# Optimization experiments

Measured on AMD Instinct MI355X. Metric: run time of the kernel, lower is better.

Reference implementation:

```python
import jax, jax.numpy as jnp
import numpy as np

B, S, C = 16, 2048, 512
E = S            # embed_dim == seq_len (RMSNorm applied on transposed seq axis)
H = 4 * E        # FFN hidden
LAMBDA_INIT = float(0.8 - 0.6 * np.exp(-0.3 * 1.0))  # layer_index = 1
SCALE = E ** (-0.25)
K = 5            # decomposition moving-average kernel


def rmsnorm(x, w, eps=1e-8):
    return x * jax.lax.rsqrt(jnp.mean(x * x, axis=-1, keepdims=True) + eps) * w


def decompose(a):
    # DLinear-style series decomposition: replicate-padded moving average along seq
    pad = (K - 1) // 2
    ap = jnp.concatenate([jnp.repeat(a[:, :1], pad, axis=1), a, jnp.repeat(a[:, -1:], pad, axis=1)], axis=1)
    n = a.shape[1]
    trend = sum(ap[:, i:i + n] for i in range(K)) / K
    return trend, a - trend


def setup_inputs() -> dict:
    key = jax.random.key(0)
    ks = jax.random.split(key, 12)
    p = lambda i, shape, s=0.02: jax.random.normal(ks[i], shape, jnp.float32) * s
    return {
        "x": jax.random.normal(ks[0], (B, S, C), jnp.float32),
        "ln_attn_w": jnp.ones((E,), jnp.float32),
        "q12_w": p(1, (E, 2 * E)), "q12_b": jnp.zeros((2 * E,), jnp.float32),
        "k12_w": p(2, (E, 2 * E)), "k12_b": jnp.zeros((2 * E,), jnp.float32),
        "v_w": p(3, (E, E)), "v_b": jnp.zeros((E,), jnp.float32),
        "lambda_q1": p(4, (E,), 0.1), "lambda_k1": p(5, (E,), 0.1),
        "lambda_q2": p(6, (E,), 0.1), "lambda_k2": p(7, (E,), 0.1),
        "norm_w": jnp.ones((E,), jnp.float32),
        "ln_ff_w": jnp.ones((E,), jnp.float32),
        "ff_w1": p(8, (E, H)), "ff_b1": jnp.zeros((H,), jnp.float32),
        "ff_w2": p(9, (H, E)), "ff_b2": jnp.zeros((E,), jnp.float32),
    }


def reference(x, ln_attn_w, q12_w, q12_b, k12_w, k12_b, v_w, v_b,
              lambda_q1, lambda_k1, lambda_q2, lambda_k2,
              norm_w, ln_ff_w, ff_w1, ff_b1, ff_w2, ff_b2):
    # pre-attention RMSNorm over the seq axis (via transpose)
    a = jnp.swapaxes(rmsnorm(jnp.swapaxes(x, -1, -2), ln_attn_w), -1, -2)  # [B,S,C]
    trend, seasonal = decompose(a)
    # project seq dim of trend/seasonal (iTransformer style: channels are tokens)
    q = jnp.swapaxes(trend, -1, -2) @ q12_w + q12_b      # [B,C,2S]
    q1, q2 = jnp.split(q, 2, axis=-1)                    # [B,C,S] each
    k = jnp.swapaxes(seasonal, -1, -2) @ k12_w + k12_b   # [B,C,2S]
    k1, k2 = jnp.split(k, 2, axis=-1)                    # [B,C,S]
    v = jnp.swapaxes(a, -1, -2) @ v_w + v_b              # [B,C,S]
    a1 = jnp.einsum('bis,bjs->bij', q1, k1) * SCALE      # [B,C,C]
    a2 = jnp.einsum('bis,bjs->bij', q2, k2) * SCALE      # [B,C,C]
    lam = jnp.exp(jnp.sum(lambda_q1 * lambda_k1)) - jnp.exp(jnp.sum(lambda_q2 * lambda_k2)) + LAMBDA_INIT
    d = jax.nn.softmax(a1, axis=-1) - lam * jax.nn.softmax(a2, axis=-1)
    attn = rmsnorm(d @ v, norm_w) * (1.0 - LAMBDA_INIT)  # [B,C,S]
    x = x + jnp.swapaxes(attn, -1, -2)
    # FFN over the seq axis
    h = rmsnorm(jnp.swapaxes(x, -1, -2), ln_ff_w)        # [B,C,S]
    ff = jax.nn.gelu(h @ ff_w1 + ff_b1, approximate=False) @ ff_w2 + ff_b2
    return x + jnp.swapaxes(ff, -1, -2)
```

## Files before the change

kernel.cpp:

```cpp
#include <hip/hip_runtime.h>
#include <hip/hip_bf16.h>

#define B_ 16
#define S_ 2048
#define C_ 512
#define H_ 8192

#define LAMBDA_INIT_F 0.3555090675909693f
#define ONE_M_LI_F    0.6444909324090307f
#define SCALE_F       0.14865088937534013f

using bf16x8 = __attribute__((ext_vector_type(8))) short;
using f32x4  = __attribute__((ext_vector_type(4))) float;

__device__ __forceinline__ float b2f(ushort u) {
  union { unsigned u; float f; } x; x.u = ((unsigned)u) << 16; return x.f;
}
__device__ __forceinline__ ushort f2b(float f) {
  union { float f; unsigned u; } x; x.f = f;
  unsigned r = x.u + 0x7fffu + ((x.u >> 16) & 1u);
  return (ushort)(r >> 16);
}

__device__ __forceinline__ void load_lds16(const void* g, void* s) {
  __builtin_amdgcn_global_load_lds((const __attribute__((address_space(1))) void*)g,
                                   (__attribute__((address_space(3))) void*)s,
                                   16, 0, 0);
}

#define WAITV8() asm volatile("s_waitcnt vmcnt(8)" ::: "memory")
#define WAITV4() asm volatile("s_waitcnt vmcnt(4)" ::: "memory")
#define WAITV0() asm volatile("s_waitcnt vmcnt(0)" ::: "memory")
#define WAITL0() do { asm volatile("s_waitcnt lgkmcnt(0)" ::: "memory"); __builtin_amdgcn_sched_barrier(0); } while (0)
#define BAR()    __builtin_amdgcn_s_barrier()

template <int EPI>
__global__ __launch_bounds__(512, 1) void gemm256(
    const ushort* __restrict__ A, const ushort* __restrict__ Bt,
    ushort* __restrict__ C, const float* __restrict__ bias,
    const ushort* __restrict__ addm,
    int K, int lda, int ldb, int ldc)
{
  __shared__ ushort lds[65536];
  const int t = threadIdx.x, w = t >> 6, lane = t & 63;
  const int fr = lane & 15, khl = lane >> 4;
  const int wr = w >> 2, wc = w & 3;

  const int gx = gridDim.x, gy = gridDim.y;
  const int id = blockIdx.y * gx + blockIdx.x;
  const int xcd = id & 7, l = id >> 3;
  const int tnb = (gy == 16) ? 3 : 2;
  const int lm = l >> tnb, ln = l & ((1 << tnb) - 1);
  const int m0 = ((xcd & 3) * 8 + lm) * 256;
  const int n0 = ((xcd >> 2) * (1 << tnb) + ln) * 256;

  const int sl    = (t & 7) ^ ((t >> 3) & 7);
  const int rbase = ((t >> 3) << 1) + (sl >> 2);
  const int khs   = sl & 3;
  const size_t aoff = (size_t)(m0 + rbase) * lda + khs * 8;
  const size_t boff = (size_t)(n0 + rbase) * ldb + khs * 8;
  const size_t jstA = (size_t)128 * lda, jstB = (size_t)128 * ldb;

  int ao[8], bo[4];
#pragma unroll
  for (int m = 0; m < 8; ++m) {
    const int row = wr * 128 + m * 16 + fr, dr = row >> 1;
    const int so = (((row & 1) << 2) + khl) ^ (dr & 7);
    ao[m] = dr * 64 + so * 8;
  }
#pragma unroll
  for (int n = 0; n < 4; ++n) {
    const int row = wc * 64 + n * 16 + fr, dr = row >> 1;
    const int so = (((row & 1) << 2) + khl) ^ (dr & 7);
    bo[n] = 8192 + dr * 64 + so * 8;
  }

  f32x4 acc[8][4] = {};
  const int U = K >> 5;

#define STAGE_U(u) do { \
    const ushort* sa_ = A  + aoff + (size_t)(u) * 32; \
    const ushort* sb_ = Bt + boff + (size_t)(u) * 32; \
    ushort* da_ = &lds[((u) & 3) * 16384 + w * 512]; \
    load_lds16(sa_, da_); load_lds16(sa_ + jstA, da_ + 4096); \
    load_lds16(sb_, da_ + 8192); load_lds16(sb_ + jstB, da_ + 12288); } while (0)
#define LDFRAG(u) do { const int sb_ = ((u) & 3) * 16384; \
    _Pragma("unroll") for (int m_ = 0; m_ < 8; ++m_) af[m_] = *(const bf16x8*)&lds[sb_ + ao[m_]]; \
    _Pragma("unroll") for (int n_ = 0; n_ < 4; ++n_) bg[n_] = *(const bf16x8*)&lds[sb_ + bo[n_]]; } while (0)
#define MFMA32() do { __builtin_amdgcn_s_setprio(1); \
    _Pragma("unroll") for (int m_ = 0; m_ < 8; ++m_) \
    _Pragma("unroll") for (int n_ = 0; n_ < 4; ++n_) \
      acc[m_][n_] = __builtin_amdgcn_mfma_f32_16x16x32_bf16(af[m_], bg[n_], acc[m_][n_], 0, 0, 0); \
    __builtin_amdgcn_s_setprio(0); } while (0)

  STAGE_U(0); STAGE_U(1); STAGE_U(2);
  WAITV8(); BAR();

  bf16x8 af[8], bg[4];
#pragma unroll 4
  for (int u = 0; u <= U - 4; ++u) {
    LDFRAG(u);
    STAGE_U(u + 3);
    WAITL0();
    MFMA32();
    WAITV8();
    BAR();
  }
  {
    LDFRAG(U - 3);
    WAITL0();
    MFMA32();
    WAITV4();
    BAR();
  }
  {
    LDFRAG(U - 2);
    WAITL0();
    MFMA32();
    WAITV0();
    BAR();
  }
  {
    LDFRAG(U - 1);
    WAITL0();
    MFMA32();
  }
#undef STAGE_U
#undef LDFRAG
#undef MFMA32

  const int r0 = khl * 4;
#pragma unroll
  for (int m = 0; m < 8; ++m)
#pragma unroll
    for (int nf = 0; nf < 4; ++nf) {
      const int gr = m0 + wr * 128 + m * 16 + r0;
      const int gc = n0 + wc * 64 + nf * 16 + fr;
      const float bb = (EPI == 3) ? 0.f : bias[gc];
#pragma unroll
      for (int r = 0; r < 4; ++r) {
        const size_t idx = (size_t)(gr + r) * ldc + gc;
        float v = acc[m][nf][r];
        if constexpr (EPI == 1) v += bb;
        if constexpr (EPI == 2) { v += bb; v = 0.5f * v * (1.f + erff(v * 0.7071067811865475f)); }
        if constexpr (EPI == 4) v += bb + b2f(addm[idx]) + b2f(C[idx]);
        C[idx] = f2b(v);
      }
    }
}

template <int EPI>
__global__ __launch_bounds__(256, 2) void gemm_nt(
    const ushort* __restrict__ Aall, const ushort* __restrict__ Ball,
    void* __restrict__ Call, int K, int lda, int ldb, int ldc,
    long sA, long sB, long sC, long sA2, long sB2, float alpha)
{
  __shared__ ushort lA[4096];
  __shared__ ushort lB[4096];
  const int t = threadIdx.x;
  const int m0 = blockIdx.x * 128, n0 = blockIdx.y * 128;
  const int zb = blockIdx.z & 15, zh = blockIdx.z >> 4;
  const ushort* A  = Aall + (size_t)zb * sA + (size_t)zh * sA2;
  const ushort* Bt = Ball + (size_t)zb * sB + (size_t)zh * sB2;
  const int lane = t & 63;
  const int wave = t >> 6;
  const int wm = (wave >> 1) * 64, wn = (wave & 1) * 64;
  const int fr = lane & 15, kh = lane >> 4;
  f32x4 acc[4][4] = {};
  const int srow = t >> 2;
  const int scol = (t & 3) * 8;
  const size_t ar0 = (size_t)(m0 + srow) * lda + scol;
  const size_t ar1 = (size_t)(m0 + 64 + srow) * lda + scol;
  const size_t br0 = (size_t)(n0 + srow) * ldb + scol;
  const size_t br1 = (size_t)(n0 + 64 + srow) * ldb + scol;
  const int wbase = wave * 512;

  for (int k0 = 0; k0 < K; k0 += 32) {
    __syncthreads();
    load_lds16(A + ar0 + k0,  &lA[wbase]);
    load_lds16(A + ar1 + k0,  &lA[2048 + wbase]);
    load_lds16(Bt + br0 + k0, &lB[wbase]);
    load_lds16(Bt + br1 + k0, &lB[2048 + wbase]);
    __syncthreads();
    bf16x8 af[4], bg[4];
#pragma unroll
    for (int i = 0; i < 4; ++i)
      af[i] = *(const bf16x8*)&lA[(wm + i * 16 + fr) * 32 + kh * 8];
#pragma unroll
    for (int j = 0; j < 4; ++j)
      bg[j] = *(const bf16x8*)&lB[(wn + j * 16 + fr) * 32 + kh * 8];
#pragma unroll
    for (int i = 0; i < 4; ++i)
#pragma unroll
      for (int j = 0; j < 4; ++j)
        acc[i][j] = __builtin_amdgcn_mfma_f32_16x16x32_bf16(af[i], bg[j], acc[i][j], 0, 0, 0);
  }

  const int r0 = kh * 4;
  if constexpr (EPI == 0) {
    float* C = (float*)Call + (size_t)blockIdx.z * sC;
#pragma unroll
    for (int i = 0; i < 4; ++i)
#pragma unroll
      for (int j = 0; j < 4; ++j) {
        const int gr = m0 + wm + i * 16 + r0;
        const int gc = n0 + wn + j * 16 + fr;
#pragma unroll
        for (int r = 0; r < 4; ++r)
          C[(size_t)(gr + r) * ldc + gc] = acc[i][j][r] * alpha;
      }
  } else {
    ushort* C = (ushort*)Call + (size_t)blockIdx.z * sC;
#pragma unroll
    for (int i = 0; i < 4; ++i)
#pragma unroll
      for (int j = 0; j < 4; ++j) {
        const int gr = m0 + wm + i * 16 + r0;
        const int gc = n0 + wn + j * 16 + fr;
#pragma unroll
        for (int r = 0; r < 4; ++r)
          C[(size_t)(gr + r) * ldc + gc] = f2b(acc[i][j][r] * alpha);
      }
  }
}

__device__ __forceinline__ float block_sum(float v, float* red) {
#pragma unroll
  for (int o = 32; o > 0; o >>= 1) v += __shfl_down(v, o, 64);
  __syncthreads();
  if ((threadIdx.x & 63) == 0) red[threadIdx.x >> 6] = v;
  __syncthreads();
  return red[0] + red[1] + red[2] + red[3];
}
__device__ __forceinline__ float block_max(float v, float* red) {
#pragma unroll
  for (int o = 32; o > 0; o >>= 1) v = fmaxf(v, __shfl_down(v, o, 64));
  __syncthreads();
  if ((threadIdx.x & 63) == 0) red[threadIdx.x >> 6] = v;
  __syncthreads();
  return fmaxf(fmaxf(red[0], red[1]), fmaxf(red[2], red[3]));
}

__global__ __launch_bounds__(256) void k_rms_part(const float* __restrict__ x, float* __restrict__ part) {
  const int c = blockIdx.x * 256 + threadIdx.x;
  const int sl = blockIdx.y;
  const int b = blockIdx.z;
  const float* p = x + (size_t)b * S_ * C_ + c;
  const int s0 = sl * 256;
  float s = 0.f;
  for (int i = 0; i < 256; ++i) { float v = p[(size_t)(s0 + i) * C_]; s += v * v; }
  part[((size_t)b * C_ + c) * 8 + sl] = s;
}
__global__ __launch_bounds__(256) void k_rms_fin(const float* __restrict__ part, float* __restrict__ rms1) {
  const int i = blockIdx.x * 256 + threadIdx.x;
  const float* p = part + (size_t)i * 8;
  float s = 0.f;
#pragma unroll
  for (int j = 0; j < 8; ++j) s += p[j];
  rms1[i] = rsqrtf(s * (1.f / S_) + 1e-8f);
}

__global__ __launch_bounds__(256) void k_trans_norm(const float* __restrict__ x, const float* __restrict__ rms1,
                                                    const float* __restrict__ w,
                                                    ushort* __restrict__ aT, ushort* __restrict__ xT) {
  __shared__ float tile[32][33];
  const int s0 = blockIdx.x * 32, c0 = blockIdx.y * 32, b = blockIdx.z;
  const int tx = threadIdx.x, ty = threadIdx.y;
  const float* xb = x + (size_t)b * S_ * C_;
#pragma unroll
  for (int r = 0; r < 4; ++r) {
    const int s = ty + 8 * r;
    tile[s][tx] = xb[(size_t)(s0 + s) * C_ + c0 + tx];
  }
  __syncthreads();
#pragma unroll
  for (int r = 0; r < 4; ++r) {
    const int c = ty + 8 * r;
    const float v = tile[tx][c];
    const float rm = rms1[b * C_ + c0 + c];
    const size_t o = ((size_t)b * C_ + c0 + c) * S_ + s0 + tx;
    xT[o] = f2b(v);
    aT[o] = f2b(v * rm * w[s0 + tx]);
  }
}

__global__ __launch_bounds__(256) void k_wtrans(const float* __restrict__ W, ushort* __restrict__ WT,
                                                int Kd, int Ndstride, int n_base) {
  __shared__ float tile[32][33];
  const int k0 = blockIdx.x * 32, n0 = blockIdx.y * 32;
  const int tx = threadIdx.x, ty = threadIdx.y;
#pragma unroll
  for (int r = 0; r < 4; ++r) {
    const int k = ty + 8 * r;
    tile[k][tx] = W[(size_t)(k0 + k) * Ndstride + n_base + n0 + tx];
  }
  __syncthreads();
#pragma unroll
  for (int r = 0; r < 4; ++r) {
    const int n = ty + 8 * r;
    WT[(size_t)(n0 + n) * Kd + k0 + tx] = f2b(tile[tx][n]);
  }
}

__global__ __launch_bounds__(256) void k_bt(const ushort* __restrict__ in, ushort* __restrict__ out, int R, int CL) {
  __shared__ ushort tile[32][33];
  const int r0 = blockIdx.x * 32, c0 = blockIdx.y * 32;
  const size_t zb = (size_t)blockIdx.z * R * CL;
  const int tx = threadIdx.x, ty = threadIdx.y;
#pragma unroll
  for (int r = 0; r < 4; ++r) {
    const int rr = ty + 8 * r;
    tile[rr][tx] = in[zb + (size_t)(r0 + rr) * CL + c0 + tx];
  }
  __syncthreads();
#pragma unroll
  for (int r = 0; r < 4; ++r) {
    const int cc = ty + 8 * r;
    out[zb + (size_t)(c0 + cc) * R + r0 + tx] = tile[tx][cc];
  }
}

__device__ __forceinline__ float trend5(const ushort* p, int s) {
  float sum = 0.f;
#pragma unroll
  for (int d = -2; d <= 2; ++d) {
    int ss = s + d; ss = ss < 0 ? 0 : (ss > S_ - 1 ? S_ - 1 : ss);
    sum += b2f(p[ss]);
  }
  return sum * 0.2f;
}
__global__ __launch_bounds__(256) void k_decomp2(const ushort* __restrict__ aT,
                                                 ushort* __restrict__ trT, ushort* __restrict__ seT) {
  const size_t i = (size_t)blockIdx.x * 256 + threadIdx.x;
  const int s = (int)(i & (S_ - 1));
  const ushort* p = aT + (i - s);
  const float tr = trend5(p, s);
  trT[i] = f2b(tr);
  seT[i] = f2b(b2f(p[s]) - tr);
}

__global__ __launch_bounds__(256) void k_lambda(const float* __restrict__ lq1, const float* __restrict__ lk1,
                                                const float* __restrict__ lq2, const float* __restrict__ lk2,
                                                float* __restrict__ lam) {
  __shared__ float r1[4], r2[4];
  const int t = threadIdx.x;
  float s1 = 0.f, s2 = 0.f;
  for (int i = t; i < S_; i += 256) { s1 += lq1[i] * lk1[i]; s2 += lq2[i] * lk2[i]; }
#pragma unroll
  for (int o = 32; o > 0; o >>= 1) { s1 += __shfl_down(s1, o, 64); s2 += __shfl_down(s2, o, 64); }
  if ((t & 63) == 0) { r1[t >> 6] = s1; r2[t >> 6] = s2; }
  __syncthreads();
  if (t == 0) {
    const float a = r1[0] + r1[1] + r1[2] + r1[3];
    const float b = r2[0] + r2[1] + r2[2] + r2[3];
    *lam = expf(a) - expf(b) + LAMBDA_INIT_F;
  }
}

__global__ __launch_bounds__(256) void k_softmax(const float* __restrict__ a1, const float* __restrict__ a2,
                                                 const float* __restrict__ lamp, ushort* __restrict__ dm) {
  __shared__ float red[4];
  const size_t row = blockIdx.x;
  const float* p1 = a1 + row * 512;
  const float* p2 = a2 + row * 512;
  const int t = threadIdx.x;
  const float v1a = p1[t], v1b = p1[t + 256];
  const float v2a = p2[t], v2b = p2[t + 256];
  const float m1 = block_max(fmaxf(v1a, v1b), red);
  const float m2 = block_max(fmaxf(v2a, v2b), red);
  const float e1a = expf(v1a - m1), e1b = expf(v1b - m1);
  const float e2a = expf(v2a - m2), e2b = expf(v2b - m2);
  const float s1 = block_sum(e1a + e1b, red);
  const float s2 = block_sum(e2a + e2b, red);
  const float i1 = 1.f / s1, i2 = (*lamp) / s2;
  ushort* o = dm + row * 512;
  o[t]       = f2b(e1a * i1 - e2a * i2);
  o[t + 256] = f2b(e1b * i1 - e2b * i2);
}

__global__ __launch_bounds__(256) void k_postattn(const ushort* __restrict__ P, const ushort* __restrict__ xT,
                                                  const float* __restrict__ norm_w, const float* __restrict__ ln_ff_w,
                                                  ushort* __restrict__ attn, ushort* __restrict__ h) {
  __shared__ float red[4];
  const size_t row = blockIdx.x;
  const ushort* p = P + row * S_;
  const int t = threadIdx.x;
  float v[8]; float ss = 0.f;
#pragma unroll
  for (int i = 0; i < 8; ++i) { v[i] = b2f(p[t + 256 * i]); ss += v[i] * v[i]; }
  ss = block_sum(ss, red);
  const float inv = rsqrtf(ss * (1.f / S_) + 1e-8f);
  const ushort* xr = xT + row * S_;
  ushort* ar = attn + row * S_;
  float x2[8]; float ss2 = 0.f;
#pragma unroll
  for (int i = 0; i < 8; ++i) {
    const int s = t + 256 * i;
    const float at = v[i] * inv * norm_w[s] * ONE_M_LI_F;
    ar[s] = f2b(at);
    const float xx = b2f(xr[s]) + at;
    x2[i] = xx; ss2 += xx * xx;
  }
  ss2 = block_sum(ss2, red);
  const float inv2 = rsqrtf(ss2 * (1.f / S_) + 1e-8f);
  ushort* hr = h + row * S_;
#pragma unroll
  for (int i = 0; i < 8; ++i) { const int s = t + 256 * i; hr[s] = f2b(x2[i] * inv2 * ln_ff_w[s]); }
}

__global__ __launch_bounds__(256) void k_final2(const float* __restrict__ x, const ushort* __restrict__ sumT,
                                                float* __restrict__ out) {
  __shared__ float tile[32][33];
  const int s0 = blockIdx.x * 32, c0 = blockIdx.y * 32, b = blockIdx.z;
  const int tx = threadIdx.x, ty = threadIdx.y;
#pragma unroll
  for (int r = 0; r < 4; ++r) {
    const int c = ty + 8 * r;
    tile[c][tx] = b2f(sumT[((size_t)b * C_ + c0 + c) * S_ + s0 + tx]);
  }
  __syncthreads();
#pragma unroll
  for (int r = 0; r < 4; ++r) {
    const int s = ty + 8 * r;
    const size_t o = ((size_t)b * S_ + s0 + s) * C_ + c0 + tx;
    out[o] = x[o] + tile[tx][s];
  }
}

__global__ void k_probe(float* out, float v) { out[0] = v; }

extern "C" void kernel_launch(void* const* d_in, const int* in_sizes, int n_in,
                              void* d_out, int out_size, void* d_ws, size_t ws_size,
                              hipStream_t stream) {
  const float* x       = (const float*)d_in[0];
  const float* ln_attn = (const float*)d_in[1];
  const float* q12_w   = (const float*)d_in[2];
  const float* q12_b   = (const float*)d_in[3];
  const float* k12_w   = (const float*)d_in[4];
  const float* k12_b   = (const float*)d_in[5];
  const float* v_w     = (const float*)d_in[6];
  const float* v_b     = (const float*)d_in[7];
  const float* lq1     = (const float*)d_in[8];
  const float* lk1     = (const float*)d_in[9];
  const float* lq2     = (const float*)d_in[10];
  const float* lk2     = (const float*)d_in[11];
  const float* norm_w  = (const float*)d_in[12];
  const float* ln_ff   = (const float*)d_in[13];
  const float* ff_w1   = (const float*)d_in[14];
  const float* ff_b1   = (const float*)d_in[15];
  const float* ff_w2   = (const float*)d_in[16];
  const float* ff_b2   = (const float*)d_in[17];
  float* out = (float*)d_out;

  if (ws_size < 184844544ull) {
    k_probe<<<1, 1, 0, stream>>>(out, (float)(ws_size >> 20));
    return;
  }

  char* ws = (char*)d_ws;
  ushort* slotA = (ushort*)(ws + 0);
  ushort* slotB = (ushort*)(ws + 33554432);
  ushort* slotC = (ushort*)(ws + 67108864);
  ushort* slotD = (ushort*)(ws + 100663296);
  ushort* slotE = (ushort*)(ws + 134217728);
  ushort* slotF = (ushort*)(ws + 167772160);
  float*  part  = (float*) (ws + 184549376);
  float*  rms1  = (float*) (ws + 184811520);
  float*  lamp  = (float*) (ws + 184844288);

  ushort* aT   = slotA;
  ushort* xT   = slotE;
  ushort* Vm   = slotB;
  ushort* VT   = slotD;
  ushort* trT  = slotB;
  ushort* seT  = slotC;
  ushort* K12  = slotA;
  float*  scr  = (float*)slotC;
  ushort* Pm   = slotB;
  ushort* attn = slotC;
  ushort* hbuf = slotA;
  ushort* ff1T = slotB;
  ushort* ff2T = slotD;
  ushort* ffo  = slotE;
  ushort* wsl  = slotF;
  ushort* dmat = slotF;
  ushort* Qm   = (ushort*)d_out;
  ushort* H1   = (ushort*)d_out;

  const dim3 blk256(256), blk512(512), blkT(32, 8);

  k_rms_part<<<dim3(2, 8, B_), blk256, 0, stream>>>(x, part);
  k_rms_fin<<<dim3(32), blk256, 0, stream>>>(part, rms1);
  k_trans_norm<<<dim3(64, 16, B_), blkT, 0, stream>>>(x, rms1, ln_attn, aT, xT);

  k_wtrans<<<dim3(64, 64), blkT, 0, stream>>>(v_w, wsl, 2048, 2048, 0);
  gemm256<1><<<dim3(32, 8), blk512, 0, stream>>>(aT, wsl, Vm, v_b, nullptr, 2048, 2048, 2048, 2048);
  k_bt<<<dim3(16, 64, B_), blkT, 0, stream>>>(Vm, VT, 512, 2048);

  k_decomp2<<<dim3(65536), blk256, 0, stream>>>(aT, trT, seT);

  k_wtrans<<<dim3(64, 128), blkT, 0, stream>>>(q12_w, wsl, 2048, 4096, 0);
  gemm256<1><<<dim3(32, 16), blk512, 0, stream>>>(trT, wsl, Qm, q12_b, nullptr, 2048, 2048, 2048, 4096);

  k_lambda<<<dim3(1), blk256, 0, stream>>>(lq1, lk1, lq2, lk2, lamp);
  k_wtrans<<<dim3(64, 128), blkT, 0, stream>>>(k12_w, wsl, 2048, 4096, 0);
  gemm256<1><<<dim3(32, 16), blk512, 0, stream>>>(seT, wsl, K12, k12_b, nullptr, 2048, 2048, 2048, 4096);

  gemm_nt<0><<<dim3(4, 4, 32), blk256, 0, stream>>>(Qm, K12, scr, 2048, 4096, 4096, 512,
                                                    512L * 4096, 512L * 4096, 512L * 512,
                                                    2048L, 2048L, SCALE_F);

  k_softmax<<<dim3(8192), blk256, 0, stream>>>(scr, scr + 4194304, lamp, dmat);
  gemm_nt<3><<<dim3(4, 16, B_), blk256, 0, stream>>>(dmat, VT, Pm, 512, 512, 512, 2048,
                                                     512L * 512, 2048L * 512, 512L * 2048,
                                                     0, 0, 1.f);

  k_postattn<<<dim3(8192), blk256, 0, stream>>>(Pm, xT, norm_w, ln_ff, attn, hbuf);

  k_wtrans<<<dim3(64, 256), blkT, 0, stream>>>(ff_w1, ff1T, 2048, 8192, 0);
  k_wtrans<<<dim3(256, 64), blkT, 0, stream>>>(ff_w2, ff2T, 8192, 2048, 0);

  gemm256<2><<<dim3(32, 16), blk512, 0, stream>>>(hbuf, ff1T, H1, ff_b1, nullptr,
                                                  2048, 2048, 2048, 4096);
  gemm256<3><<<dim3(32, 8), blk512, 0, stream>>>(H1, ff2T, ffo, nullptr, nullptr,
                                                 4096, 4096, 8192, 2048);
  gemm256<2><<<dim3(32, 16), blk512, 0, stream>>>(hbuf, ff1T + (size_t)4096 * 2048, H1,
                                                  ff_b1 + 4096, nullptr, 2048, 2048, 2048, 4096);
  gemm256<4><<<dim3(32, 8), blk512, 0, stream>>>(H1, ff2T + 4096, ffo, ff_b2, attn,
                                                 4096, 4096, 8192, 2048);

  k_final2<<<dim3(64, 16, B_), blkT, 0, stream>>>(x, ffo, out);
}
```

Baseline: 1.227 ms.

## Reassociate Q·Kᵀ through precomputed Wq·Wkᵀ and emit V transposed directly

The attention scores are computed as trend·(Wq_i·Wk_iᵀ)·seasonalᵀ, with the two 2048×2048 weight products formed once per call. This replaces the wide Q and K projections with smaller GEMMs. The q-bias contribution that varies with the key index is recovered through a matvec/gemv vector added inside the softmax; the key-bias and constant terms cancel under softmax. Separately, the V projection now writes its output in transposed layout through gemm_nt with a row-bias epilogue, which removes the separate bf16 transpose kernel. The trade-off is extra small kernels and lower numerical precision, since the weight product is rounded to bf16.

```diff
diff --git a/kernel.cpp b/kernel.cpp
--- a/kernel.cpp
+++ b/kernel.cpp
@@ -153,7 +153,8 @@
 __global__ __launch_bounds__(256, 2) void gemm_nt(
     const ushort* __restrict__ Aall, const ushort* __restrict__ Ball,
     void* __restrict__ Call, int K, int lda, int ldb, int ldc,
-    long sA, long sB, long sC, long sA2, long sB2, float alpha)
+    long sA, long sB, long sC, long sA2, long sB2, float alpha,
+    const float* __restrict__ bias)
 {
   __shared__ ushort lA[4096];
   __shared__ ushort lB[4096];
@@ -218,8 +219,12 @@
         const int gr = m0 + wm + i * 16 + r0;
         const int gc = n0 + wn + j * 16 + fr;
 #pragma unroll
-        for (int r = 0; r < 4; ++r)
-          C[(size_t)(gr + r) * ldc + gc] = f2b(acc[i][j][r] * alpha);
+        for (int r = 0; r < 4; ++r) {
+          float v = acc[i][j][r];
+          if constexpr (EPI == 3) v *= alpha;
+          if constexpr (EPI == 5) v += bias[gr + r];
+          C[(size_t)(gr + r) * ldc + gc] = f2b(v);
+        }
       }
   }
 }
@@ -302,22 +307,43 @@
   }
 }
 
-__global__ __launch_bounds__(256) void k_bt(const ushort* __restrict__ in, ushort* __restrict__ out, int R, int CL) {
-  __shared__ ushort tile[32][33];
-  const int r0 = blockIdx.x * 32, c0 = blockIdx.y * 32;
-  const size_t zb = (size_t)blockIdx.z * R * CL;
-  const int tx = threadIdx.x, ty = threadIdx.y;
-#pragma unroll
-  for (int r = 0; r < 4; ++r) {
-    const int rr = ty + 8 * r;
-    tile[rr][tx] = in[zb + (size_t)(r0 + rr) * CL + c0 + tx];
-  }
-  __syncthreads();
-#pragma unroll
-  for (int r = 0; r < 4; ++r) {
-    const int cc = ty + 8 * r;
-    out[zb + (size_t)(c0 + cc) * R + r0 + tx] = tile[tx][cc];
-  }
+__global__ __launch_bounds__(256) void k_convert(const float* __restrict__ in, ushort* __restrict__ out) {
+  const size_t i = ((size_t)blockIdx.x * 256 + threadIdx.x) * 8;
+  const f32x4 v0 = *(const f32x4*)(in + i);
+  const f32x4 v1 = *(const f32x4*)(in + i + 4);
+  bf16x8 o;
+#pragma unroll
+  for (int j = 0; j < 4; ++j) { o[j] = (short)f2b(v0[j]); o[4 + j] = (short)f2b(v1[j]); }
+  *(bf16x8*)(out + i) = o;
+}
+
+__global__ __launch_bounds__(256) void k_matvec(const float* __restrict__ kw, const float* __restrict__ qb,
+                                                float* __restrict__ vv) {
+  __shared__ float red[4];
+  const int s = blockIdx.x;
+  const float* row = kw + (size_t)s * 4096;
+  const int t = threadIdx.x;
+  float s1 = 0.f, s2 = 0.f;
+  for (int i = t; i < 2048; i += 256) { s1 += row[i] * qb[i]; s2 += row[2048 + i] * qb[2048 + i]; }
+  s1 = block_sum(s1, red);
+  s2 = block_sum(s2, red);
+  if (t == 0) { vv[s] = s1; vv[2048 + s] = s2; }
+}
+
+__global__ __launch_bounds__(256) void k_gemv(const ushort* __restrict__ seT, const float* __restrict__ vv,
+                                              float* __restrict__ rvec) {
+  __shared__ float red[4];
+  const int r = blockIdx.x;
+  const ushort* row = seT + (size_t)r * 2048;
+  const int t = threadIdx.x;
+  float s1 = 0.f, s2 = 0.f;
+  for (int i = t; i < 2048; i += 256) {
+    const float sv = b2f(row[i]);
+    s1 += sv * vv[i]; s2 += sv * vv[2048 + i];
+  }
+  s1 = block_sum(s1, red);
+  s2 = block_sum(s2, red);
+  if (t == 0) { rvec[r] = SCALE_F * s1; rvec[8192 + r] = SCALE_F * s2; }
 }
 
 __device__ __forceinline__ float trend5(const ushort* p, int s) {
@@ -358,14 +384,16 @@
 }
 
 __global__ __launch_bounds__(256) void k_softmax(const float* __restrict__ a1, const float* __restrict__ a2,
-                                                 const float* __restrict__ lamp, ushort* __restrict__ dm) {
+                                                 const float* __restrict__ lamp, const float* __restrict__ rvec,
+                                                 ushort* __restrict__ dm) {
   __shared__ float red[4];
   const size_t row = blockIdx.x;
+  const int jb = ((int)row >> 9) << 9;
   const float* p1 = a1 + row * 512;
   const float* p2 = a2 + row * 512;
   const int t = threadIdx.x;
-  const float v1a = p1[t], v1b = p1[t + 256];
-  const float v2a = p2[t], v2b = p2[t + 256];
+  const float v1a = p1[t] + rvec[jb + t],        v1b = p1[t + 256] + rvec[jb + t + 256];
+  const float v2a = p2[t] + rvec[8192 + jb + t], v2b = p2[t + 256] + rvec[8192 + jb + t + 256];
   const float m1 = block_max(fmaxf(v1a, v1b), red);
   const float m2 = block_max(fmaxf(v2a, v2b), red);
   const float e1a = expf(v1a - m1), e1b = expf(v1b - m1);
@@ -469,22 +497,25 @@
   float*  lamp  = (float*) (ws + 184844288);
 
   ushort* aT   = slotA;
+  ushort* k12c = slotA;
+  ushort* T12s = slotA;
+  ushort* hbuf = slotA;
+  ushort* trT  = slotB;
+  ushort* Pm   = slotB;
+  ushort* ff1T = slotB;
+  ushort* seT  = slotC;
+  ushort* attn = slotC;
+  ushort* VT   = slotD;
+  ushort* ff2T = slotD;
   ushort* xT   = slotE;
-  ushort* Vm   = slotB;
-  ushort* VT   = slotD;
-  ushort* trT  = slotB;
-  ushort* seT  = slotC;
-  ushort* K12  = slotA;
-  float*  scr  = (float*)slotC;
-  ushort* Pm   = slotB;
-  ushort* attn = slotC;
-  ushort* hbuf = slotA;
-  ushort* ff1T = slotB;
-  ushort* ff2T = slotD;
   ushort* ffo  = slotE;
   ushort* wsl  = slotF;
+  ushort* q12c = slotF;
   ushort* dmat = slotF;
-  ushort* Qm   = (ushort*)d_out;
+  float*  vvb  = (float*)(ws + 167772160 + 12582912);
+  float*  rvec = vvb + 4096;
+  ushort* M12T = (ushort*)d_out;
+  float*  scr  = (float*)((char*)d_out + 16777216);
   ushort* H1   = (ushort*)d_out;
 
   const dim3 blk256(256), blk512(512), blkT(32, 8);
@@ -494,26 +525,32 @@
   k_trans_norm<<<dim3(64, 16, B_), blkT, 0, stream>>>(x, rms1, ln_attn, aT, xT);
 
   k_wtrans<<<dim3(64, 64), blkT, 0, stream>>>(v_w, wsl, 2048, 2048, 0);
-  gemm256<1><<<dim3(32, 8), blk512, 0, stream>>>(aT, wsl, Vm, v_b, nullptr, 2048, 2048, 2048, 2048);
-  k_bt<<<dim3(16, 64, B_), blkT, 0, stream>>>(Vm, VT, 512, 2048);
+  gemm_nt<5><<<dim3(16, 4, 16), blk256, 0, stream>>>(wsl, aT, VT, 2048, 2048, 2048, 512,
+                                                     0, 1048576, 1048576, 0, 0, 1.f, v_b);
 
   k_decomp2<<<dim3(65536), blk256, 0, stream>>>(aT, trT, seT);
-
-  k_wtrans<<<dim3(64, 128), blkT, 0, stream>>>(q12_w, wsl, 2048, 4096, 0);
-  gemm256<1><<<dim3(32, 16), blk512, 0, stream>>>(trT, wsl, Qm, q12_b, nullptr, 2048, 2048, 2048, 4096);
-
   k_lambda<<<dim3(1), blk256, 0, stream>>>(lq1, lk1, lq2, lk2, lamp);
-  k_wtrans<<<dim3(64, 128), blkT, 0, stream>>>(k12_w, wsl, 2048, 4096, 0);
-  gemm256<1><<<dim3(32, 16), blk512, 0, stream>>>(seT, wsl, K12, k12_b, nullptr, 2048, 2048, 2048, 4096);
-
-  gemm_nt<0><<<dim3(4, 4, 32), blk256, 0, stream>>>(Qm, K12, scr, 2048, 4096, 4096, 512,
-                                                    512L * 4096, 512L * 4096, 512L * 512,
-                                                    2048L, 2048L, SCALE_F);
-
-  k_softmax<<<dim3(8192), blk256, 0, stream>>>(scr, scr + 4194304, lamp, dmat);
+
+  k_convert<<<dim3(4096), blk256, 0, stream>>>(q12_w, q12c);
+  k_convert<<<dim3(4096), blk256, 0, stream>>>(k12_w, k12c);
+  gemm_nt<3><<<dim3(16, 16, 2), blk256, 0, stream>>>(k12c, q12c, M12T, 2048, 4096, 4096, 2048,
+                                                     2048, 2048, 4194304, 0, 0, 1.f, nullptr);
+
+  k_matvec<<<dim3(2048), blk256, 0, stream>>>(k12_w, q12_b, vvb);
+  k_gemv<<<dim3(8192), blk256, 0, stream>>>(seT, vvb, rvec);
+
+  gemm256<3><<<dim3(32, 8), blk512, 0, stream>>>(trT, M12T, T12s, nullptr, nullptr,
+                                                 2048, 2048, 2048, 2048);
+  gemm_nt<0><<<dim3(4, 4, 16), blk256, 0, stream>>>(T12s, seT, scr, 2048, 2048, 2048, 512,
+                                                    1048576, 1048576, 262144, 0, 0, SCALE_F, nullptr);
+  gemm256<3><<<dim3(32, 8), blk512, 0, stream>>>(trT, M12T + 4194304, T12s, nullptr, nullptr,
+                                                 2048, 2048, 2048, 2048);
+  gemm_nt<0><<<dim3(4, 4, 16), blk256, 0, stream>>>(T12s, seT, scr + 4194304, 2048, 2048, 2048, 512,
+                                                    1048576, 1048576, 262144, 0, 0, SCALE_F, nullptr);
+
+  k_softmax<<<dim3(8192), blk256, 0, stream>>>(scr, scr + 4194304, lamp, rvec, dmat);
   gemm_nt<3><<<dim3(4, 16, B_), blk256, 0, stream>>>(dmat, VT, Pm, 512, 512, 512, 2048,
-                                                     512L * 512, 2048L * 512, 512L * 2048,
-                                                     0, 0, 1.f);
+                                                     262144, 1048576, 1048576, 0, 0, 1.f, nullptr);
 
   k_postattn<<<dim3(8192), blk256, 0, stream>>>(Pm, xT, norm_w, ln_ff, attn, hbuf);
 
```

After: 1.183 ms. -3.6%, faster.
